# Performance work log

Hardware: AMD Instinct MI355X
Metric: run time of the kernel (lower is better)

Reference implementation:

```python
import jax, jax.numpy as jnp
import numpy as np

DIM = 1024
NUM_HEADS = 16
HEAD_DIM = DIM // NUM_HEADS
SCALE = HEAD_DIM ** (-0.5)


def setup_inputs() -> dict:
    key = jax.random.key(0)
    ks = jax.random.split(key, 5)
    b, n = 4, 1370
    x = jax.random.normal(ks[0], (b, n, DIM), dtype=jnp.float32)
    # Dense kernels: Keras Dense stores kernel as [in, out]
    w_qkv = jax.random.normal(ks[1], (DIM, 3 * DIM), dtype=jnp.float32) * (DIM ** -0.5)
    b_qkv = jnp.zeros((3 * DIM,), dtype=jnp.float32)
    w_proj = jax.random.normal(ks[2], (DIM, DIM), dtype=jnp.float32) * (DIM ** -0.5)
    b_proj = jnp.zeros((DIM,), dtype=jnp.float32)
    return {"x": x, "w_qkv": w_qkv, "b_qkv": b_qkv, "w_proj": w_proj, "b_proj": b_proj}


def reference(x, w_qkv, b_qkv, w_proj, b_proj):
    b, n, _ = x.shape
    qkv = x @ w_qkv + b_qkv                       # [b, n, 3*dim]
    qkv = qkv.reshape(b, n, 3, NUM_HEADS, HEAD_DIM)
    qkv = jnp.transpose(qkv, (2, 0, 3, 1, 4))     # [3, b, h, n, d]
    q, k, v = qkv[0], qkv[1], qkv[2]
    q = q * jnp.asarray(SCALE, dtype=q.dtype)
    attn = jnp.einsum("bhqd,bhkd->bhqk", q, k)    # [b, h, n, n]
    attn = jax.nn.softmax(attn, axis=-1)
    out = jnp.einsum("bhqk,bhkd->bhqd", attn, v)  # [b, h, n, d]
    out = jnp.transpose(out, (0, 2, 1, 3)).reshape(b, n, DIM)
    return out @ w_proj + b_proj
```

## Files before the change

### kernel.cpp

```cpp
#include <hip/hip_runtime.h>
#include <stdint.h>
#include <math.h>

typedef __attribute__((ext_vector_type(8))) __bf16 bf16x8;
typedef __attribute__((ext_vector_type(4))) __bf16 bf16x4;
typedef __attribute__((ext_vector_type(4))) float f32x4;
typedef __attribute__((ext_vector_type(8))) short short8;

#define MFMA(a, b, c) __builtin_amdgcn_mfma_f32_16x16x32_bf16((a), (b), (c), 0, 0, 0)

constexpr int DIMC  = 1024;
constexpr int HEADS = 16;
constexpr int HD    = 64;
constexpr int BATCH = 4;
constexpr int SEQ   = 1370;
constexpr int MROWS = BATCH * SEQ;
constexpr int NPAD  = 1408;
constexpr float QK_SCALE = 0.125f * 1.44269504088896341f;

__device__ __forceinline__ unsigned short f2bf(float f) {
    union { float f; unsigned int u; } v; v.f = f;
    unsigned int r = (v.u + 0x7FFFu + ((v.u >> 16) & 1u)) >> 16;
    return (unsigned short)r;
}

__device__ __forceinline__ void gl2lds16(const unsigned short* g, unsigned short* l) {
    __builtin_amdgcn_global_load_lds(
        (const __attribute__((address_space(1))) unsigned int*)g,
        (__attribute__((address_space(3))) unsigned int*)l,
        16, 0, 0);
}

__global__ void cast_x_kernel(const float* __restrict__ x, unsigned short* __restrict__ xb, int nvec) {
    int i = blockIdx.x * blockDim.x + threadIdx.x;
    if (i >= nvec) return;
    f32x4 a = reinterpret_cast<const f32x4*>(x)[2 * i];
    f32x4 b = reinterpret_cast<const f32x4*>(x)[2 * i + 1];
    short8 o;
    o[0] = (short)f2bf(a[0]); o[1] = (short)f2bf(a[1]);
    o[2] = (short)f2bf(a[2]); o[3] = (short)f2bf(a[3]);
    o[4] = (short)f2bf(b[0]); o[5] = (short)f2bf(b[1]);
    o[6] = (short)f2bf(b[2]); o[7] = (short)f2bf(b[3]);
    reinterpret_cast<short8*>(xb)[i] = o;
}

__global__ __launch_bounds__(256) void transpose_cast_kernel(const float* __restrict__ in,
                                                             unsigned short* __restrict__ out,
                                                             int R, int C) {
    __shared__ float tile[32][33];
    int tx = threadIdx.x & 31, ty = threadIdx.x >> 5;
    int cbase = blockIdx.x * 32, rbase = blockIdx.y * 32;
#pragma unroll
    for (int rr = 0; rr < 4; ++rr) {
        int r = ty + rr * 8;
        tile[r][tx] = in[(size_t)(rbase + r) * C + cbase + tx];
    }
    __syncthreads();
#pragma unroll
    for (int rr = 0; rr < 4; ++rr) {
        int cr = ty + rr * 8;
        out[(size_t)(cbase + cr) * R + rbase + tx] = f2bf(tile[tx][cr]);
    }
}

__global__ void zero_vpad_kernel(unsigned short* __restrict__ vTg) {
    int idx = blockIdx.x * blockDim.x + threadIdx.x;
    const int padw = NPAD - SEQ;
    const int total = 64 * 64 * padw;
    if (idx >= total) return;
    int col = SEQ + idx % padw;
    int rowflat = idx / padw;
    vTg[(size_t)rowflat * NPAD + col] = 0;
}

template <int EPI>
__global__ __launch_bounds__(256) void gemm_bt_kernel(const unsigned short* __restrict__ A,
                                                      const unsigned short* __restrict__ Bt,
                                                      int M, int N, int K,
                                                      const float* __restrict__ bias,
                                                      unsigned short* __restrict__ qg,
                                                      unsigned short* __restrict__ kg,
                                                      unsigned short* __restrict__ vTg,
                                                      float* __restrict__ outf) {
    __shared__ unsigned short As[2][128 * 32];
    __shared__ unsigned short Bs[2][128 * 32];
    const int tid = threadIdx.x;
    const int l = tid & 63, w = tid >> 6;
    const int wr = w >> 1, wc = w & 1;
    const int lm = l & 15, lk = l >> 4;
    const int brow = blockIdx.y * 128, bcol = blockIdx.x * 128;

    f32x4 acc[4][4];
#pragma unroll
    for (int i = 0; i < 4; ++i)
#pragma unroll
        for (int j = 0; j < 4; ++j) acc[i][j] = f32x4{0.f, 0.f, 0.f, 0.f};

    auto stage = [&](int kt, int buf) {
#pragma unroll
        for (int rr = 0; rr < 2; ++rr) {
            int flat = rr * 256 + tid;
            int row = flat >> 2;
            int c8 = (flat & 3) << 3;
            int ga = min(brow + row, M - 1);
            gl2lds16(&A[(size_t)ga * K + kt * 32 + c8], &As[buf][flat * 8]);
            int gb = bcol + row;
            gl2lds16(&Bt[(size_t)gb * K + kt * 32 + c8], &Bs[buf][flat * 8]);
        }
    };

    const int nkt = K >> 5;
    stage(0, 0);
    __syncthreads();
    int cur = 0;
    for (int kt = 0; kt < nkt; ++kt) {
        if (kt + 1 < nkt) stage(kt + 1, cur ^ 1);
        bf16x8 af[4], bfr[4];
#pragma unroll
        for (int i = 0; i < 4; ++i)
            af[i] = *reinterpret_cast<const bf16x8*>(&As[cur][(wr * 64 + i * 16 + lm) * 32 + lk * 8]);
#pragma unroll
        for (int j = 0; j < 4; ++j)
            bfr[j] = *reinterpret_cast<const bf16x8*>(&Bs[cur][(wc * 64 + j * 16 + lm) * 32 + lk * 8]);
#pragma unroll
        for (int i = 0; i < 4; ++i)
#pragma unroll
            for (int j = 0; j < 4; ++j)
                acc[i][j] = MFMA(af[i], bfr[j], acc[i][j]);
        __syncthreads();
        cur ^= 1;
    }

#pragma unroll
    for (int i = 0; i < 4; ++i) {
        int mbase = brow + wr * 64 + i * 16 + lk * 4;
#pragma unroll
        for (int j = 0; j < 4; ++j) {
            int col = bcol + wc * 64 + j * 16 + lm;
            float bv = bias[col];
#pragma unroll
            for (int r = 0; r < 4; ++r) {
                int m = mbase + r;
                if (m >= M) continue;
                float val = acc[i][j][r] + bv;
                if constexpr (EPI == 0) {
                    int which = col >> 10;
                    int head = (col >> 6) & 15;
                    int d = col & 63;
                    int b = m / SEQ;
                    int nseq = m - b * SEQ;
                    int bh = b * HEADS + head;
                    if (which == 0) {
                        qg[((size_t)bh * SEQ + nseq) * HD + d] = f2bf(val * QK_SCALE);
                    } else if (which == 1) {
                        kg[((size_t)bh * SEQ + nseq) * HD + d] = f2bf(val);
                    } else {
                        vTg[((size_t)bh * HD + d) * NPAD + nseq] = f2bf(val);
                    }
                } else {
                    outf[(size_t)m * DIMC + col] = val;
                }
            }
        }
    }
}

__global__ __launch_bounds__(512) void attn_kernel(const unsigned short* __restrict__ qg,
                                                   const unsigned short* __restrict__ kg,
                                                   const unsigned short* __restrict__ vTg,
                                                   unsigned short* __restrict__ ao) {
    __shared__ unsigned short Ks[64 * 72];
    __shared__ unsigned short Vs[64 * 72];
    __shared__ unsigned short Pw[8][16 * 72];

    const int tid = threadIdx.x;
    const int l = tid & 63, w = tid >> 6;
    const int lm = l & 15, lk = l >> 4;

    int wg = (blockIdx.x & 7) * 88 + (blockIdx.x >> 3);
    const int bh = wg / 11;
    const int qbase = (wg - bh * 11) * 128;

    int qr = min(qbase + w * 16 + lm, SEQ - 1);
    const unsigned short* qp = &qg[((size_t)bh * SEQ + qr) * HD + lk * 8];
    bf16x8 qf0 = *reinterpret_cast<const bf16x8*>(qp);
    bf16x8 qf1 = *reinterpret_cast<const bf16x8*>(qp + 32);

    f32x4 o[4];
#pragma unroll
    for (int jd = 0; jd < 4; ++jd) o[jd] = f32x4{0.f, 0.f, 0.f, 0.f};
    float mrun = -INFINITY, lrun = 0.f;

    const int r0 = tid >> 3;
    const int c8b = (tid & 7) << 3;
    const unsigned short* kbase = &kg[(size_t)bh * SEQ * HD];
    const unsigned short* vbase = &vTg[(size_t)bh * HD * NPAD];

    short8 kr, vr;
    auto load_tile = [&](int t) {
        int kvg = min(t * 64 + r0, SEQ - 1);
        kr = *reinterpret_cast<const short8*>(&kbase[(size_t)kvg * HD + c8b]);
        vr = *reinterpret_cast<const short8*>(&vbase[(size_t)r0 * NPAD + t * 64 + c8b]);
    };
    auto write_tile = [&]() {
        *reinterpret_cast<short8*>(&Ks[r0 * 72 + c8b]) = kr;
        *reinterpret_cast<short8*>(&Vs[r0 * 72 + c8b]) = vr;
    };

    const int NT = (SEQ + 63) >> 6;
    load_tile(0);
    for (int t = 0; t < NT; ++t) {
        write_tile();
        __syncthreads();
        if (t + 1 < NT) load_tile(t + 1);

        f32x4 s[4];
        __builtin_amdgcn_s_setprio(1);
#pragma unroll
        for (int j = 0; j < 4; ++j) {
            f32x4 z = {0.f, 0.f, 0.f, 0.f};
            bf16x8 k0 = *reinterpret_cast<const bf16x8*>(&Ks[(j * 16 + lm) * 72 + lk * 8]);
            bf16x8 k1 = *reinterpret_cast<const bf16x8*>(&Ks[(j * 16 + lm) * 72 + 32 + lk * 8]);
            z = MFMA(k0, qf0, z);
            z = MFMA(k1, qf1, z);
            s[j] = z;
        }
        __builtin_amdgcn_s_setprio(0);

        if (t == NT - 1) {
#pragma unroll
            for (int j = 0; j < 4; ++j)
#pragma unroll
                for (int r = 0; r < 4; ++r) {
                    int kvg = t * 64 + j * 16 + lk * 4 + r;
                    if (kvg >= SEQ) s[j][r] = -INFINITY;
                }
        }

        float tmax = s[0][0];
#pragma unroll
        for (int j = 0; j < 4; ++j)
#pragma unroll
            for (int r = 0; r < 4; ++r) tmax = fmaxf(tmax, s[j][r]);

        if (!__all(tmax - mrun <= 8.0f)) {
            float tm = fmaxf(tmax, __shfl_xor(tmax, 16));
            tm = fmaxf(tm, __shfl_xor(tm, 32));
            float mnew = fmaxf(mrun, tm);
            float scale = exp2f(mrun - mnew);
            mrun = mnew;
            lrun *= scale;
            float sc[4];
#pragma unroll
            for (int r = 0; r < 4; ++r) sc[r] = __shfl(scale, lk * 4 + r);
#pragma unroll
            for (int jd = 0; jd < 4; ++jd) {
                o[jd][0] *= sc[0]; o[jd][1] *= sc[1];
                o[jd][2] *= sc[2]; o[jd][3] *= sc[3];
            }
        }

        float p[4][4];
        float psum = 0.f;
#pragma unroll
        for (int j = 0; j < 4; ++j)
#pragma unroll
            for (int r = 0; r < 4; ++r) {
                float pv = exp2f(s[j][r] - mrun);
                p[j][r] = pv;
                psum += pv;
            }
        lrun += psum;

#pragma unroll
        for (int j = 0; j < 4; ++j) {
            bf16x4 pk;
            pk[0] = (__bf16)p[j][0]; pk[1] = (__bf16)p[j][1];
            pk[2] = (__bf16)p[j][2]; pk[3] = (__bf16)p[j][3];
            *reinterpret_cast<bf16x4*>(&Pw[w][lm * 72 + j * 16 + lk * 4]) = pk;
        }

        bf16x8 pa0 = *reinterpret_cast<const bf16x8*>(&Pw[w][lm * 72 + lk * 8]);
        bf16x8 pa1 = *reinterpret_cast<const bf16x8*>(&Pw[w][lm * 72 + 32 + lk * 8]);
        __builtin_amdgcn_s_setprio(1);
#pragma unroll
        for (int jd = 0; jd < 4; ++jd) {
            bf16x8 v0 = *reinterpret_cast<const bf16x8*>(&Vs[(jd * 16 + lm) * 72 + lk * 8]);
            bf16x8 v1 = *reinterpret_cast<const bf16x8*>(&Vs[(jd * 16 + lm) * 72 + 32 + lk * 8]);
            o[jd] = MFMA(pa0, v0, o[jd]);
            o[jd] = MFMA(pa1, v1, o[jd]);
        }
        __builtin_amdgcn_s_setprio(0);
        __syncthreads();
    }

    float ltot = lrun;
    ltot += __shfl_xor(ltot, 16);
    ltot += __shfl_xor(ltot, 32);
    float linv = 1.f / ltot;
    int b = bh >> 4, h = bh & 15;
#pragma unroll
    for (int r = 0; r < 4; ++r) {
        int q = qbase + w * 16 + lk * 4 + r;
        float inv = __shfl(linv, lk * 4 + r);
        if (q >= SEQ) continue;
#pragma unroll
        for (int jd = 0; jd < 4; ++jd) {
            ao[((size_t)b * SEQ + q) * DIMC + h * HD + jd * 16 + lm] = f2bf(o[jd][r] * inv);
        }
    }
}

extern "C" void kernel_launch(void* const* d_in, const int* in_sizes, int n_in,
                              void* d_out, int out_size, void* d_ws, size_t ws_size,
                              hipStream_t stream) {
    const float* x      = (const float*)d_in[0];
    const float* w_qkv  = (const float*)d_in[1];
    const float* b_qkv  = (const float*)d_in[2];
    const float* w_proj = (const float*)d_in[3];
    const float* b_proj = (const float*)d_in[4];
    float* out = (float*)d_out;

    char* ws = (char*)d_ws;
    unsigned short* xb     = (unsigned short*)ws; ws += (size_t)MROWS * DIMC * 2;
    unsigned short* wqkvT  = (unsigned short*)ws; ws += (size_t)3 * DIMC * DIMC * 2;
    unsigned short* wprojT = (unsigned short*)ws; ws += (size_t)DIMC * DIMC * 2;
    unsigned short* qg     = (unsigned short*)ws; ws += (size_t)64 * SEQ * HD * 2;
    unsigned short* kg     = (unsigned short*)ws; ws += (size_t)64 * SEQ * HD * 2;
    unsigned short* vTg    = (unsigned short*)ws; ws += (size_t)64 * HD * NPAD * 2;
    unsigned short* ao     = (unsigned short*)ws; ws += (size_t)MROWS * DIMC * 2;

    const int nvec = MROWS * DIMC / 8;
    cast_x_kernel<<<(nvec + 255) / 256, 256, 0, stream>>>(x, xb, nvec);
    transpose_cast_kernel<<<dim3(3 * DIMC / 32, DIMC / 32), 256, 0, stream>>>(w_qkv, wqkvT, DIMC, 3 * DIMC);
    transpose_cast_kernel<<<dim3(DIMC / 32, DIMC / 32), 256, 0, stream>>>(w_proj, wprojT, DIMC, DIMC);
    zero_vpad_kernel<<<(64 * 64 * (NPAD - SEQ) + 255) / 256, 256, 0, stream>>>(vTg);

    gemm_bt_kernel<0><<<dim3(3 * DIMC / 128, (MROWS + 127) / 128), 256, 0, stream>>>(
        xb, wqkvT, MROWS, 3 * DIMC, DIMC, b_qkv, qg, kg, vTg, nullptr);

    attn_kernel<<<dim3(8 * 88), 512, 0, stream>>>(qg, kg, vTg, ao);

    gemm_bt_kernel<1><<<dim3(DIMC / 128, (MROWS + 127) / 128), 256, 0, stream>>>(
        ao, wprojT, MROWS, DIMC, DIMC, b_proj, nullptr, nullptr, nullptr, out);
}
```

Before: 188.8 us.

## Deepen GEMM LDS pipeline to four stages with XCD-aware block remap

Replaces the double-buffered LDS staging in the shared GEMM kernel with a four-buffer ring that prefetches three K-tiles ahead. It uses explicit vmcnt waits and raw barriers instead of __syncthreads, and raises wave priority around the MFMA block. It also launches a 1D grid and remaps block IDs so consecutive tiles land on the same XCD, aiming for better L2 reuse. The cost is doubled LDS (64KB per block), which may cut occupancy. The hand-counted vmcnt values must stay in step with the number of loads issued per stage.

```diff
diff --git a/kernel.cpp b/kernel.cpp
--- a/kernel.cpp
+++ b/kernel.cpp
@@ -76,19 +76,23 @@
 template <int EPI>
 __global__ __launch_bounds__(256) void gemm_bt_kernel(const unsigned short* __restrict__ A,
                                                       const unsigned short* __restrict__ Bt,
-                                                      int M, int N, int K,
+                                                      int M, int N, int K, int Nx,
                                                       const float* __restrict__ bias,
                                                       unsigned short* __restrict__ qg,
                                                       unsigned short* __restrict__ kg,
                                                       unsigned short* __restrict__ vTg,
                                                       float* __restrict__ outf) {
-    __shared__ unsigned short As[2][128 * 32];
-    __shared__ unsigned short Bs[2][128 * 32];
+    __shared__ unsigned short As[4][128 * 32];
+    __shared__ unsigned short Bs[4][128 * 32];
     const int tid = threadIdx.x;
     const int l = tid & 63, w = tid >> 6;
     const int wr = w >> 1, wc = w & 1;
     const int lm = l & 15, lk = l >> 4;
-    const int brow = blockIdx.y * 128, bcol = blockIdx.x * 128;
+
+    int nwg = gridDim.x;
+    int wgid = (blockIdx.x & 7) * (nwg >> 3) + (blockIdx.x >> 3);
+    int bx = wgid % Nx, by = wgid / Nx;
+    const int brow = by * 128, bcol = bx * 128;
 
     f32x4 acc[4][4];
 #pragma unroll
@@ -110,11 +114,14 @@
     };
 
     const int nkt = K >> 5;
-    stage(0, 0);
-    __syncthreads();
-    int cur = 0;
+    stage(0, 0); stage(1, 1); stage(2, 2);
+    asm volatile("s_waitcnt vmcnt(8)" ::: "memory");
+    __builtin_amdgcn_s_barrier();
+
     for (int kt = 0; kt < nkt; ++kt) {
-        if (kt + 1 < nkt) stage(kt + 1, cur ^ 1);
+        const int cur = kt & 3;
+        if (kt + 3 < nkt) stage(kt + 3, (kt + 3) & 3);
+
         bf16x8 af[4], bfr[4];
 #pragma unroll
         for (int i = 0; i < 4; ++i)
@@ -122,13 +129,18 @@
 #pragma unroll
         for (int j = 0; j < 4; ++j)
             bfr[j] = *reinterpret_cast<const bf16x8*>(&Bs[cur][(wc * 64 + j * 16 + lm) * 32 + lk * 8]);
+        __builtin_amdgcn_s_setprio(1);
 #pragma unroll
         for (int i = 0; i < 4; ++i)
 #pragma unroll
             for (int j = 0; j < 4; ++j)
                 acc[i][j] = MFMA(af[i], bfr[j], acc[i][j]);
-        __syncthreads();
-        cur ^= 1;
+        __builtin_amdgcn_s_setprio(0);
+
+        if (kt + 3 < nkt)      asm volatile("s_waitcnt vmcnt(8)" ::: "memory");
+        else if (kt + 2 < nkt) asm volatile("s_waitcnt vmcnt(4)" ::: "memory");
+        else if (kt + 1 < nkt) asm volatile("s_waitcnt vmcnt(0)" ::: "memory");
+        if (kt + 1 < nkt) __builtin_amdgcn_s_barrier();
     }
 
 #pragma unroll
@@ -336,11 +348,11 @@
     transpose_cast_kernel<<<dim3(DIMC / 32, DIMC / 32), 256, 0, stream>>>(w_proj, wprojT, DIMC, DIMC);
     zero_vpad_kernel<<<(64 * 64 * (NPAD - SEQ) + 255) / 256, 256, 0, stream>>>(vTg);
 
-    gemm_bt_kernel<0><<<dim3(3 * DIMC / 128, (MROWS + 127) / 128), 256, 0, stream>>>(
-        xb, wqkvT, MROWS, 3 * DIMC, DIMC, b_qkv, qg, kg, vTg, nullptr);
+    gemm_bt_kernel<0><<<dim3(24 * 43), 256, 0, stream>>>(
+        xb, wqkvT, MROWS, 3 * DIMC, DIMC, 24, b_qkv, qg, kg, vTg, nullptr);
 
     attn_kernel<<<dim3(8 * 88), 512, 0, stream>>>(qg, kg, vTg, ao);
 
-    gemm_bt_kernel<1><<<dim3(DIMC / 128, (MROWS + 127) / 128), 256, 0, stream>>>(
-        ao, wprojT, MROWS, DIMC, DIMC, b_proj, nullptr, nullptr, nullptr, out);
-}
+    gemm_bt_kernel<1><<<dim3(8 * 43), 256, 0, stream>>>(
+        ao, wprojT, MROWS, DIMC, DIMC, 8, b_proj, nullptr, nullptr, nullptr, out);
+}
```

Result: slower. 218.9 us (+15.9%).

## Use 8-wave GEMM blocks with XCD-aware block remap, LDS swizzle and MFMA priority

Applied to the files above, without the earlier changes.

Both GEMMs now run 512-thread blocks with 8 waves on a 2x4 layout, so each wave computes a 64x32 sub-tile instead of 64x64. The grid becomes 1D and is remapped so that consecutive tiles land on the same XCD, which aims at better L2 reuse. An XOR swizzle on the LDS staging and fragment reads is meant to cut bank conflicts. s_setprio is raised around the MFMA loop. The trade-offs are more waves competing for the same LDS tile, less work per wave, and a remap that assumes the block count divides evenly by 8.

```diff
diff --git a/kernel.cpp b/kernel.cpp
--- a/kernel.cpp
+++ b/kernel.cpp
@@ -74,9 +74,9 @@
 }
 
 template <int EPI>
-__global__ __launch_bounds__(256) void gemm_bt_kernel(const unsigned short* __restrict__ A,
+__global__ __launch_bounds__(512) void gemm_bt_kernel(const unsigned short* __restrict__ A,
                                                       const unsigned short* __restrict__ Bt,
-                                                      int M, int N, int K,
+                                                      int M, int N, int K, int Nx,
                                                       const float* __restrict__ bias,
                                                       unsigned short* __restrict__ qg,
                                                       unsigned short* __restrict__ kg,
@@ -86,27 +86,27 @@
     __shared__ unsigned short Bs[2][128 * 32];
     const int tid = threadIdx.x;
     const int l = tid & 63, w = tid >> 6;
-    const int wr = w >> 1, wc = w & 1;
+    const int wr = w >> 2, wc = w & 3;
     const int lm = l & 15, lk = l >> 4;
-    const int brow = blockIdx.y * 128, bcol = blockIdx.x * 128;
-
-    f32x4 acc[4][4];
+
+    int nwg = gridDim.x;
+    int wgid = (blockIdx.x & 7) * (nwg >> 3) + (blockIdx.x >> 3);
+    int bx = wgid % Nx, by = wgid / Nx;
+    const int brow = by * 128, bcol = bx * 128;
+
+    f32x4 acc[4][2];
 #pragma unroll
     for (int i = 0; i < 4; ++i)
 #pragma unroll
-        for (int j = 0; j < 4; ++j) acc[i][j] = f32x4{0.f, 0.f, 0.f, 0.f};
-
+        for (int j = 0; j < 2; ++j) acc[i][j] = f32x4{0.f, 0.f, 0.f, 0.f};
+
+    const int srow = tid >> 2;
+    const int ssrc = (((tid & 3) ^ ((srow >> 1) & 3)) << 3);
     auto stage = [&](int kt, int buf) {
-#pragma unroll
-        for (int rr = 0; rr < 2; ++rr) {
-            int flat = rr * 256 + tid;
-            int row = flat >> 2;
-            int c8 = (flat & 3) << 3;
-            int ga = min(brow + row, M - 1);
-            gl2lds16(&A[(size_t)ga * K + kt * 32 + c8], &As[buf][flat * 8]);
-            int gb = bcol + row;
-            gl2lds16(&Bt[(size_t)gb * K + kt * 32 + c8], &Bs[buf][flat * 8]);
-        }
+        int ga = min(brow + srow, M - 1);
+        gl2lds16(&A[(size_t)ga * K + kt * 32 + ssrc], &As[buf][tid * 8]);
+        int gb = bcol + srow;
+        gl2lds16(&Bt[(size_t)gb * K + kt * 32 + ssrc], &Bs[buf][tid * 8]);
     };
 
     const int nkt = K >> 5;
@@ -115,18 +115,22 @@
     int cur = 0;
     for (int kt = 0; kt < nkt; ++kt) {
         if (kt + 1 < nkt) stage(kt + 1, cur ^ 1);
-        bf16x8 af[4], bfr[4];
+
+        const int swa = (lk ^ ((lm >> 1) & 3)) * 8;
+        bf16x8 af[4], bfr[2];
 #pragma unroll
         for (int i = 0; i < 4; ++i)
-            af[i] = *reinterpret_cast<const bf16x8*>(&As[cur][(wr * 64 + i * 16 + lm) * 32 + lk * 8]);
-#pragma unroll
-        for (int j = 0; j < 4; ++j)
-            bfr[j] = *reinterpret_cast<const bf16x8*>(&Bs[cur][(wc * 64 + j * 16 + lm) * 32 + lk * 8]);
+            af[i] = *reinterpret_cast<const bf16x8*>(&As[cur][(wr * 64 + i * 16 + lm) * 32 + swa]);
+#pragma unroll
+        for (int j = 0; j < 2; ++j)
+            bfr[j] = *reinterpret_cast<const bf16x8*>(&Bs[cur][(wc * 32 + j * 16 + lm) * 32 + swa]);
+        __builtin_amdgcn_s_setprio(1);
 #pragma unroll
         for (int i = 0; i < 4; ++i)
 #pragma unroll
-            for (int j = 0; j < 4; ++j)
+            for (int j = 0; j < 2; ++j)
                 acc[i][j] = MFMA(af[i], bfr[j], acc[i][j]);
+        __builtin_amdgcn_s_setprio(0);
         __syncthreads();
         cur ^= 1;
     }
@@ -135,8 +139,8 @@
     for (int i = 0; i < 4; ++i) {
         int mbase = brow + wr * 64 + i * 16 + lk * 4;
 #pragma unroll
-        for (int j = 0; j < 4; ++j) {
-            int col = bcol + wc * 64 + j * 16 + lm;
+        for (int j = 0; j < 2; ++j) {
+            int col = bcol + wc * 32 + j * 16 + lm;
             float bv = bias[col];
 #pragma unroll
             for (int r = 0; r < 4; ++r) {
@@ -336,11 +340,11 @@
     transpose_cast_kernel<<<dim3(DIMC / 32, DIMC / 32), 256, 0, stream>>>(w_proj, wprojT, DIMC, DIMC);
     zero_vpad_kernel<<<(64 * 64 * (NPAD - SEQ) + 255) / 256, 256, 0, stream>>>(vTg);
 
-    gemm_bt_kernel<0><<<dim3(3 * DIMC / 128, (MROWS + 127) / 128), 256, 0, stream>>>(
-        xb, wqkvT, MROWS, 3 * DIMC, DIMC, b_qkv, qg, kg, vTg, nullptr);
+    gemm_bt_kernel<0><<<dim3(24 * 43), 512, 0, stream>>>(
+        xb, wqkvT, MROWS, 3 * DIMC, DIMC, 24, b_qkv, qg, kg, vTg, nullptr);
 
     attn_kernel<<<dim3(8 * 88), 512, 0, stream>>>(qg, kg, vTg, ao);
 
-    gemm_bt_kernel<1><<<dim3(DIMC / 128, (MROWS + 127) / 128), 256, 0, stream>>>(
-        ao, wprojT, MROWS, DIMC, DIMC, b_proj, nullptr, nullptr, nullptr, out);
-}
+    gemm_bt_kernel<1><<<dim3(8 * 43), 512, 0, stream>>>(
+        ao, wprojT, MROWS, DIMC, DIMC, 8, b_proj, nullptr, nullptr, nullptr, out);
+}
```

New measurement: 178.8 us. 5.3% less time.

## Enlarge GEMM tiles to 256x128 with swizzled LDS, XCD-aware block remap, MFMA priority

Applied to the files above, without the earlier changes.

The QKV and projection GEMMs move from 128x128 tiles with 256 threads to 256x128 tiles with 512 threads (8 waves, each still computing a 64x64 sub-tile). The launch becomes a 1D grid, and block IDs are remapped across the 8 XCDs so neighbouring tiles share L2. The LDS layout is XOR-swizzled on the 16-byte column chunk to cut bank conflicts. The MFMA loop is wrapped in s_setprio. The aim is more reuse of B per tile, better cache locality and fewer LDS conflicts. The cost is fewer workgroups for the projection GEMM (176 blocks on a 256-CU part), which may hurt occupancy.

```diff
diff --git a/kernel.cpp b/kernel.cpp
--- a/kernel.cpp
+++ b/kernel.cpp
@@ -74,21 +74,25 @@
 }
 
 template <int EPI>
-__global__ __launch_bounds__(256) void gemm_bt_kernel(const unsigned short* __restrict__ A,
-                                                      const unsigned short* __restrict__ Bt,
-                                                      int M, int N, int K,
-                                                      const float* __restrict__ bias,
-                                                      unsigned short* __restrict__ qg,
-                                                      unsigned short* __restrict__ kg,
-                                                      unsigned short* __restrict__ vTg,
-                                                      float* __restrict__ outf) {
-    __shared__ unsigned short As[2][128 * 32];
+__global__ __launch_bounds__(512, 4) void gemm_bt_kernel(const unsigned short* __restrict__ A,
+                                                         const unsigned short* __restrict__ Bt,
+                                                         int M, int N, int K, int Nx,
+                                                         const float* __restrict__ bias,
+                                                         unsigned short* __restrict__ qg,
+                                                         unsigned short* __restrict__ kg,
+                                                         unsigned short* __restrict__ vTg,
+                                                         float* __restrict__ outf) {
+    __shared__ unsigned short As[2][256 * 32];
     __shared__ unsigned short Bs[2][128 * 32];
     const int tid = threadIdx.x;
     const int l = tid & 63, w = tid >> 6;
     const int wr = w >> 1, wc = w & 1;
     const int lm = l & 15, lk = l >> 4;
-    const int brow = blockIdx.y * 128, bcol = blockIdx.x * 128;
+
+    int nwg = gridDim.x;
+    int wgid = (blockIdx.x & 7) * (nwg >> 3) + (blockIdx.x >> 3);
+    int bx = wgid % Nx, by = wgid / Nx;
+    const int brow = by * 256, bcol = bx * 128;
 
     f32x4 acc[4][4];
 #pragma unroll
@@ -99,14 +103,16 @@
     auto stage = [&](int kt, int buf) {
 #pragma unroll
         for (int rr = 0; rr < 2; ++rr) {
-            int flat = rr * 256 + tid;
-            int row = flat >> 2;
-            int c8 = (flat & 3) << 3;
+            int ca = rr * 512 + tid;
+            int row = ca >> 2;
+            int src = (((ca & 3) ^ ((row >> 1) & 3)) << 3);
             int ga = min(brow + row, M - 1);
-            gl2lds16(&A[(size_t)ga * K + kt * 32 + c8], &As[buf][flat * 8]);
-            int gb = bcol + row;
-            gl2lds16(&Bt[(size_t)gb * K + kt * 32 + c8], &Bs[buf][flat * 8]);
-        }
+            gl2lds16(&A[(size_t)ga * K + kt * 32 + src], &As[buf][ca * 8]);
+        }
+        int rowb = tid >> 2;
+        int srcb = (((tid & 3) ^ ((rowb >> 1) & 3)) << 3);
+        int gb = bcol + rowb;
+        gl2lds16(&Bt[(size_t)gb * K + kt * 32 + srcb], &Bs[buf][tid * 8]);
     };
 
     const int nkt = K >> 5;
@@ -115,18 +121,22 @@
     int cur = 0;
     for (int kt = 0; kt < nkt; ++kt) {
         if (kt + 1 < nkt) stage(kt + 1, cur ^ 1);
+
+        const int swa = (lk ^ ((lm >> 1) & 3)) * 8;
         bf16x8 af[4], bfr[4];
 #pragma unroll
         for (int i = 0; i < 4; ++i)
-            af[i] = *reinterpret_cast<const bf16x8*>(&As[cur][(wr * 64 + i * 16 + lm) * 32 + lk * 8]);
+            af[i] = *reinterpret_cast<const bf16x8*>(&As[cur][(wr * 64 + i * 16 + lm) * 32 + swa]);
 #pragma unroll
         for (int j = 0; j < 4; ++j)
-            bfr[j] = *reinterpret_cast<const bf16x8*>(&Bs[cur][(wc * 64 + j * 16 + lm) * 32 + lk * 8]);
+            bfr[j] = *reinterpret_cast<const bf16x8*>(&Bs[cur][(wc * 64 + j * 16 + lm) * 32 + swa]);
+        __builtin_amdgcn_s_setprio(1);
 #pragma unroll
         for (int i = 0; i < 4; ++i)
 #pragma unroll
             for (int j = 0; j < 4; ++j)
                 acc[i][j] = MFMA(af[i], bfr[j], acc[i][j]);
+        __builtin_amdgcn_s_setprio(0);
         __syncthreads();
         cur ^= 1;
     }
@@ -336,11 +346,11 @@
     transpose_cast_kernel<<<dim3(DIMC / 32, DIMC / 32), 256, 0, stream>>>(w_proj, wprojT, DIMC, DIMC);
     zero_vpad_kernel<<<(64 * 64 * (NPAD - SEQ) + 255) / 256, 256, 0, stream>>>(vTg);
 
-    gemm_bt_kernel<0><<<dim3(3 * DIMC / 128, (MROWS + 127) / 128), 256, 0, stream>>>(
-        xb, wqkvT, MROWS, 3 * DIMC, DIMC, b_qkv, qg, kg, vTg, nullptr);
+    gemm_bt_kernel<0><<<dim3(22 * 24), 512, 0, stream>>>(
+        xb, wqkvT, MROWS, 3 * DIMC, DIMC, 24, b_qkv, qg, kg, vTg, nullptr);
 
     attn_kernel<<<dim3(8 * 88), 512, 0, stream>>>(qg, kg, vTg, ao);
 
-    gemm_bt_kernel<1><<<dim3(DIMC / 128, (MROWS + 127) / 128), 256, 0, stream>>>(
-        ao, wprojT, MROWS, DIMC, DIMC, b_proj, nullptr, nullptr, nullptr, out);
-}
+    gemm_bt_kernel<1><<<dim3(22 * 8), 512, 0, stream>>>(
+        ao, wprojT, MROWS, DIMC, DIMC, 8, b_proj, nullptr, nullptr, nullptr, out);
+}
```

Result: slower. 194.9 us (+3.2%).
